# Performance work log

Measured on AMD Instinct MI355X. Metric: run time of the kernel, lower is better.

The kernel has to match this reference:

```python
import jax, jax.numpy as jnp
import numpy as np

D_MODEL = 1024
NHEAD = 16
HEAD_DIM = D_MODEL // NHEAD
MLP_DIM = 4096
ROPE_THETA = 10000.0


def layer_norm(x, g, b, eps=1e-5):
    mu = jnp.mean(x, axis=-1, keepdims=True)
    var = jnp.var(x, axis=-1, keepdims=True)
    return (x - mu) * jax.lax.rsqrt(var + eps) * g + b


def rope_cos_sin(seq_len, dim):
    # lucidrains RotaryEmbedding: inv_freq over even indices, freqs repeated interleaved
    inv_freq = 1.0 / (ROPE_THETA ** (jnp.arange(0, dim, 2, dtype=jnp.float32) / dim))
    t = jnp.arange(seq_len, dtype=jnp.float32)
    freqs = t[:, None] * inv_freq[None, :]            # (S, dim/2)
    freqs = jnp.repeat(freqs, 2, axis=-1)             # (S, dim) interleaved [f0,f0,f1,f1,...]
    return jnp.cos(freqs), jnp.sin(freqs)


def apply_rope(x, cos, sin):
    # x: (B, S, H, D); interleaved rotate_half: (x0,x1) -> (-x1, x0)
    x1 = x[..., ::2]
    x2 = x[..., 1::2]
    rot = jnp.stack([-x2, x1], axis=-1).reshape(x.shape)
    c = cos[None, :, None, :]
    s = sin[None, :, None, :]
    return x * c + rot * s


def setup_inputs() -> dict:
    key = jax.random.key(0)
    ks = jax.random.split(key, 8)
    B, S = 2, 2048
    sc = 1.0 / np.sqrt(D_MODEL)
    inputs = jax.random.normal(ks[0], (B, S, D_MODEL), dtype=jnp.float32)
    return {
        "inputs": inputs,
        "ln1_g": jnp.ones((D_MODEL,), jnp.float32),
        "ln1_b": jnp.zeros((D_MODEL,), jnp.float32),
        "Wq": jax.random.normal(ks[1], (D_MODEL, D_MODEL), jnp.float32) * sc,
        "Wk": jax.random.normal(ks[2], (D_MODEL, D_MODEL), jnp.float32) * sc,
        "Wv": jax.random.normal(ks[3], (D_MODEL, D_MODEL), jnp.float32) * sc,
        "Wo": jax.random.normal(ks[4], (D_MODEL, D_MODEL), jnp.float32) * sc,
        "ln2_g": jnp.ones((D_MODEL,), jnp.float32),
        "ln2_b": jnp.zeros((D_MODEL,), jnp.float32),
        "Wfc2": jax.random.normal(ks[5], (D_MODEL, MLP_DIM), jnp.float32) * sc,
        "bfc2": jnp.zeros((MLP_DIM,), jnp.float32),
        "Wfc3": jax.random.normal(ks[6], (MLP_DIM, D_MODEL), jnp.float32) * (1.0 / np.sqrt(MLP_DIM)),
        "bfc3": jnp.zeros((D_MODEL,), jnp.float32),
    }


def reference(inputs, ln1_g, ln1_b, Wq, Wk, Wv, Wo, ln2_g, ln2_b, Wfc2, bfc2, Wfc3, bfc3):
    B, S, _ = inputs.shape
    x = layer_norm(inputs, ln1_g, ln1_b)
    q = (x @ Wq).reshape(B, S, NHEAD, HEAD_DIM)
    k = (x @ Wk).reshape(B, S, NHEAD, HEAD_DIM)
    v = (x @ Wv).reshape(B, S, NHEAD, HEAD_DIM)
    cos, sin = rope_cos_sin(S, HEAD_DIM)
    q = apply_rope(q, cos, sin)
    k = apply_rope(k, cos, sin)
    scores = jnp.einsum('bqhd,bkhd->bhqk', q, k) / np.sqrt(HEAD_DIM)
    attn = jax.nn.softmax(scores, axis=-1)
    out = jnp.einsum('bhqk,bkhd->bqhd', attn, v).reshape(B, S, D_MODEL)
    out = out @ Wo
    mlp_in = out + inputs
    h = layer_norm(mlp_in, ln2_g, ln2_b)
    h = jax.nn.gelu(h @ Wfc2 + bfc2, approximate=False)
    h = h @ Wfc3 + bfc3
    return h + mlp_in
```

## Files before the change

kernel.cpp:

```cpp
#include <hip/hip_runtime.h>
#include <cstdint>
#include <cstddef>

typedef __bf16 bf16x8 __attribute__((ext_vector_type(8)));
typedef __bf16 bf16x4 __attribute__((ext_vector_type(4)));
typedef float  f32x4  __attribute__((ext_vector_type(4)));
typedef float  f32x16 __attribute__((ext_vector_type(16)));
typedef unsigned int u32x4 __attribute__((ext_vector_type(4)));

__device__ __forceinline__ void load16_to_lds(const void* g, void* l) {
  __builtin_amdgcn_global_load_lds(
      (const __attribute__((address_space(1))) void*)g,
      (__attribute__((address_space(3))) void*)l, 16, 0, 0);
}

__device__ __forceinline__ unsigned cvt_pk_bf16(float a, float b) {
  unsigned r;
  asm("v_cvt_pk_bf16_f32 %0, %1, %2" : "=v"(r) : "v"(a), "v"(b));
  return r;
}
__device__ __forceinline__ void permlane32_swap(unsigned &a, unsigned &b) {
  asm("v_permlane32_swap_b32 %0, %1" : "+v"(a), "+v"(b));
}

__global__ __launch_bounds__(256) void transpose_cast(
    const float* __restrict__ src, __bf16* __restrict__ dst, int K, int N)
{
  __shared__ float tile[32][33];
  const int n0 = blockIdx.x * 32, k0 = blockIdx.y * 32;
  const int tx = threadIdx.x, ty = threadIdx.y;
#pragma unroll
  for (int i = 0; i < 32; i += 8)
    tile[ty + i][tx] = src[(size_t)(k0 + ty + i) * N + n0 + tx];
  __syncthreads();
#pragma unroll
  for (int i = 0; i < 32; i += 8)
    dst[(size_t)(n0 + ty + i) * K + k0 + tx] = (__bf16)tile[tx][ty + i];
}

__global__ __launch_bounds__(256) void transpose_cast_qkv(
    const float* __restrict__ s0, const float* __restrict__ s1,
    const float* __restrict__ s2, __bf16* __restrict__ dst)
{
  __shared__ float tile[32][33];
  const float* src = blockIdx.z == 0 ? s0 : blockIdx.z == 1 ? s1 : s2;
  __bf16* d = dst + (size_t)blockIdx.z * 1024 * 1024;
  const int n0 = blockIdx.x * 32, k0 = blockIdx.y * 32;
  const int tx = threadIdx.x, ty = threadIdx.y;
#pragma unroll
  for (int i = 0; i < 32; i += 8)
    tile[ty + i][tx] = src[(size_t)(k0 + ty + i) * 1024 + n0 + tx];
  __syncthreads();
#pragma unroll
  for (int i = 0; i < 32; i += 8)
    d[(size_t)(n0 + ty + i) * 1024 + k0 + tx] = (__bf16)tile[tx][ty + i];
}

__global__ __launch_bounds__(256) void ln_kernel(
    const float* __restrict__ x, const float* __restrict__ g,
    const float* __restrict__ bta, __bf16* __restrict__ out)
{
  const int row = blockIdx.x;
  const int t = threadIdx.x;
  const float4 v = ((const float4*)(x + (size_t)row * 1024))[t];
  float s  = v.x + v.y + v.z + v.w;
  float ss = v.x * v.x + v.y * v.y + v.z * v.z + v.w * v.w;
#pragma unroll
  for (int o = 32; o > 0; o >>= 1) { s += __shfl_down(s, o); ss += __shfl_down(ss, o); }
  __shared__ float rs[4], rss[4];
  const int w = t >> 6, l = t & 63;
  if (l == 0) { rs[w] = s; rss[w] = ss; }
  __syncthreads();
  s  = rs[0] + rs[1] + rs[2] + rs[3];
  ss = rss[0] + rss[1] + rss[2] + rss[3];
  const float mu = s * (1.0f / 1024.0f);
  const float var = ss * (1.0f / 1024.0f) - mu * mu;
  const float rstd = rsqrtf(var + 1e-5f);
  const float4 gg = ((const float4*)g)[t];
  const float4 bb = ((const float4*)bta)[t];
  __bf16* o = out + (size_t)row * 1024 + t * 4;
  o[0] = (__bf16)((v.x - mu) * rstd * gg.x + bb.x);
  o[1] = (__bf16)((v.y - mu) * rstd * gg.y + bb.y);
  o[2] = (__bf16)((v.z - mu) * rstd * gg.z + bb.z);
  o[3] = (__bf16)((v.w - mu) * rstd * gg.w + bb.w);
}

enum { EPI_BF16 = 0, EPI_RES_F32 = 1, EPI_GELU_BF16 = 2, EPI_BIAS_RES_F32 = 3 };

template <int TM, int KB, int EPI>
__global__ __launch_bounds__(256, 2) void gemm_bf16(
    const __bf16* __restrict__ A, const __bf16* __restrict__ Bt,
    __bf16* __restrict__ outb, float* __restrict__ outf,
    const float* __restrict__ bias, const float* __restrict__ res,
    int M, int N, int K)
{
  constexpr int MT = TM / 32;
  constexpr int KS = KB / 32;
  __shared__ __bf16 As0[TM * KB], As1[TM * KB];
  __shared__ __bf16 Bs0[128 * KB], Bs1[128 * KB];
  const int tid  = threadIdx.x;
  const int lane = tid & 63, w = tid >> 6;
  const int wm = w >> 1, wn = w & 1;
  const int quad = lane >> 4, l16 = lane & 15;
  const int m0 = blockIdx.y * TM, n0 = blockIdx.x * 128;

  f32x4 acc[MT][4] = {};
  const __bf16* Ag = A  + (size_t)m0 * K;
  const __bf16* Bg = Bt + (size_t)n0 * K;

#define G_STAGE(AsX, BsX, k0) {                                            \
    _Pragma("unroll")                                                      \
    for (int r2 = 0; r2 < TM * KB / 2048; ++r2) {                          \
      const int c = r2 * 256 + tid;                                        \
      const int r = c / (KB / 8), cb = c % (KB / 8);                       \
      const int g = (KB == 64) ? (cb ^ (r & 7)) : cb;                      \
      load16_to_lds(Ag + (size_t)r * K + (k0) + g * 8, &AsX[c * 8]);       \
    }                                                                      \
    _Pragma("unroll")                                                      \
    for (int r2 = 0; r2 < KB / 16; ++r2) {                                 \
      const int c = r2 * 256 + tid;                                        \
      const int r = c / (KB / 8), cb = c % (KB / 8);                       \
      const int g = (KB == 64) ? (cb ^ (r & 7)) : cb;                      \
      load16_to_lds(Bg + (size_t)r * K + (k0) + g * 8, &BsX[c * 8]);       \
    } }

#define G_COMPUTE(AsX, BsX) {                                              \
    bf16x8 af[MT][KS], bfr[4][KS];                                         \
    _Pragma("unroll")                                                      \
    for (int mt = 0; mt < MT; ++mt) {                                      \
      const int row = wm * (TM / 2) + mt * 16 + l16;                       \
      _Pragma("unroll")                                                    \
      for (int ks = 0; ks < KS; ++ks) {                                    \
        const int ch = (KB == 64) ? ((ks * 4 + quad) ^ (row & 7)) : quad;  \
        af[mt][ks] = *(const bf16x8*)&AsX[row * KB + ch * 8];              \
      }                                                                    \
    }                                                                      \
    _Pragma("unroll")                                                      \
    for (int nt = 0; nt < 4; ++nt) {                                       \
      const int row = wn * 64 + nt * 16 + l16;                             \
      _Pragma("unroll")                                                    \
      for (int ks = 0; ks < KS; ++ks) {                                    \
        const int ch = (KB == 64) ? ((ks * 4 + quad) ^ (row & 7)) : quad;  \
        bfr[nt][ks] = *(const bf16x8*)&BsX[row * KB + ch * 8];             \
      }                                                                    \
    }                                                                      \
    _Pragma("unroll")                                                      \
    for (int ks = 0; ks < KS; ++ks)                                        \
      _Pragma("unroll")                                                    \
      for (int mt = 0; mt < MT; ++mt)                                      \
        _Pragma("unroll")                                                  \
        for (int nt = 0; nt < 4; ++nt)                                     \
          acc[mt][nt] = __builtin_amdgcn_mfma_f32_16x16x32_bf16(           \
              af[mt][ks], bfr[nt][ks], acc[mt][nt], 0, 0, 0);              \
  }

  G_STAGE(As0, Bs0, 0);
  const int nk = K / KB;
  for (int kt = 0; kt < nk; kt += 2) {
    __syncthreads();
    if (kt + 1 < nk) G_STAGE(As1, Bs1, (kt + 1) * KB);
    G_COMPUTE(As0, Bs0);
    __syncthreads();
    if (kt + 2 < nk) G_STAGE(As0, Bs0, (kt + 2) * KB);
    G_COMPUTE(As1, Bs1);
  }
#undef G_STAGE
#undef G_COMPUTE

#pragma unroll
  for (int mt = 0; mt < MT; ++mt) {
#pragma unroll
    for (int nt = 0; nt < 4; ++nt) {
      const int col = n0 + wn * 64 + nt * 16 + l16;
#pragma unroll
      for (int i = 0; i < 4; ++i) {
        const int row = m0 + wm * (TM / 2) + mt * 16 + quad * 4 + i;
        float v = acc[mt][nt][i];
        const size_t idx = (size_t)row * N + col;
        if (EPI == EPI_BF16) {
          outb[idx] = (__bf16)v;
        } else if (EPI == EPI_RES_F32) {
          outf[idx] = v + res[idx];
        } else if (EPI == EPI_GELU_BF16) {
          v += bias[col];
          outb[idx] = (__bf16)(0.5f * v * (1.0f + erff(v * 0.70710678118f)));
        } else {
          v += bias[col];
          outf[idx] = v + res[idx];
        }
      }
    }
  }
}

__global__ __launch_bounds__(256) void rope_qk(
    const __bf16* __restrict__ qkv, __bf16* __restrict__ qr, __bf16* __restrict__ kr)
{
  const int idx = blockIdx.x * 256 + threadIdx.x;
  const int d2 = idx & 31;
  const int h  = (idx >> 5) & 15;
  const int bs = idx >> 9;
  const int s  = bs & 2047;
  const int b  = bs >> 11;
  const float inv_freq = exp2f(-((float)d2 * (1.0f / 32.0f)) * 13.2877123795f);
  const float ang = (float)s * inv_freq;
  const float c = cosf(ang), sn = sinf(ang);
  const float QS = 0.125f * 1.44269504f;
  const __bf16* qp = qkv + (size_t)bs * 3072 + h * 64 + 2 * d2;
  const __bf16* kp = qp + 1024;
  const float q0 = (float)qp[0], q1 = (float)qp[1];
  const float k0 = (float)kp[0], k1 = (float)kp[1];
  const size_t o = ((size_t)(b * 16 + h) * 2048 + s) * 64 + 2 * d2;
  qr[o]     = (__bf16)((q0 * c - q1 * sn) * QS);
  qr[o + 1] = (__bf16)((q1 * c + q0 * sn) * QS);
  kr[o]     = (__bf16)(k0 * c - k1 * sn);
  kr[o + 1] = (__bf16)(k1 * c + k0 * sn);
}

__global__ __launch_bounds__(256) void v_transpose(
    const __bf16* __restrict__ qkv, __bf16* __restrict__ vt)
{
  __shared__ __bf16 t[64][66];
  const int st = blockIdx.x, h = blockIdx.y, b = blockIdx.z;
  const int tx = threadIdx.x & 63, ty = threadIdx.x >> 6;
  const int s0 = st * 64;
  const __bf16* src = qkv + ((size_t)(b * 2048 + s0)) * 3072 + 2048 + h * 64;
#pragma unroll
  for (int i = 0; i < 64; i += 4)
    t[ty + i][tx] = src[(size_t)(ty + i) * 3072 + tx];
  __syncthreads();
  __bf16* dst = vt + ((size_t)(b * 16 + h) * 64) * 2048 + s0;
#pragma unroll
  for (int i = 0; i < 64; i += 4)
    dst[(size_t)(ty + i) * 2048 + tx] = t[tx][ty + i];
}

__global__ __launch_bounds__(256, 2) void attn_kernel(
    const __bf16* __restrict__ qr, const __bf16* __restrict__ kr,
    const __bf16* __restrict__ vt, __bf16* __restrict__ attn_o)
{
  constexpr int S = 2048, DH = 64, NH = 16, BQ = 128, BKK = 64;
  __shared__ __align__(16) __bf16 Qs[BQ * 64];
  __shared__ __align__(16) __bf16 Ks0[64 * 64], Ks1[64 * 64], Ks2[64 * 64], Ks3[64 * 64];
  __shared__ __align__(16) __bf16 Vts0[64 * 64], Vts1[64 * 64], Vts2[64 * 64], Vts3[64 * 64];

  const int tid = threadIdx.x;
  const int lane = tid & 63, w = tid >> 6;
  const int l32 = lane & 31, half = lane >> 5;
  const int qt = blockIdx.x, h = blockIdx.y, b = blockIdx.z;
  const int bh = b * NH + h;
  const __bf16* Q  = qr + ((size_t)bh * S + qt * BQ) * DH;
  const __bf16* Kp = kr + (size_t)bh * S * DH;
  const __bf16* Vp = vt + (size_t)bh * DH * S;
  __bf16* Pb = Qs + w * 2048;

#define A_STAGE(KsX, VtsX, kk) {                                           \
    _Pragma("unroll")                                                      \
    for (int r2 = 0; r2 < 2; ++r2) {                                       \
      const int c = r2 * 256 + tid;                                        \
      const int r = c >> 3, cb = c & 7;                                    \
      const int cg = (cb ^ (r & 7)) * 8;                                   \
      load16_to_lds(Kp + (size_t)((kk) + r) * DH + cg, &KsX[c * 8]);       \
      load16_to_lds(Vp + (size_t)r * S + (kk) + cg, &VtsX[c * 8]);         \
    } }

#pragma unroll
  for (int r4 = 0; r4 < 4; ++r4) {
    const int c = r4 * 256 + tid;
    const int r = c >> 3, cb = c & 7;
    load16_to_lds(Q + (size_t)r * DH + ((cb ^ (r & 7)) * 8), &Qs[c * 8]);
  }
  A_STAGE(Ks0, Vts0, 0);
  A_STAGE(Ks1, Vts1, BKK);
  __syncthreads();

  bf16x8 qfB[4];
  {
    const int row = w * 32 + l32;
#pragma unroll
    for (int c = 0; c < 4; ++c)
      qfB[c] = *(const bf16x8*)&Qs[row * 64 + (((2 * c + half) ^ (row & 7)) * 8)];
  }

  float mreg = -3.0e38f, lreg = 0.0f;
  f32x16 oacc[2] = {};
  const f32x16 zz = {};
  f32x16 saA[2], saB[2];

#define A_QK(KsX, saX) {                                                   \
    bf16x8 kf[2][4];                                                       \
    _Pragma("unroll")                                                      \
    for (int t = 0; t < 2; ++t) {                                          \
      const int row = 32 * t + l32;                                        \
      _Pragma("unroll")                                                    \
      for (int c = 0; c < 4; ++c)                                          \
        kf[t][c] = *(const bf16x8*)&KsX[row * 64 + (((2 * c + half) ^ (l32 & 7)) * 8)]; \
    }                                                                      \
    __builtin_amdgcn_s_setprio(1);                                         \
    _Pragma("unroll")                                                      \
    for (int t = 0; t < 2; ++t) {                                          \
      saX[t] = __builtin_amdgcn_mfma_f32_32x32x16_bf16(kf[t][0], qfB[0], zz, 0, 0, 0); \
      _Pragma("unroll")                                                    \
      for (int c = 1; c < 4; ++c)                                          \
        saX[t] = __builtin_amdgcn_mfma_f32_32x32x16_bf16(kf[t][c], qfB[c], saX[t], 0, 0, 0); \
    }                                                                      \
    __builtin_amdgcn_s_setprio(0);                                         \
  }

#define A_SMPV(saC, VtsX) {                                                \
    bf16x8 vf[2][4];                                                       \
    _Pragma("unroll")                                                      \
    for (int v = 0; v < 2; ++v) {                                          \
      const int row = 32 * v + l32;                                        \
      _Pragma("unroll")                                                    \
      for (int c = 0; c < 4; ++c)                                          \
        vf[v][c] = *(const bf16x8*)&VtsX[row * 64 + (((2 * c + half) ^ (l32 & 7)) * 8)]; \
    }                                                                      \
    float pm[8];                                                           \
    _Pragma("unroll")                                                      \
    for (int t = 0; t < 2; ++t)                                            \
      _Pragma("unroll")                                                    \
      for (int g = 0; g < 4; ++g)                                          \
        pm[t * 4 + g] = fmaxf(fmaxf(saC[t][4 * g], saC[t][4 * g + 1]),     \
                              fmaxf(saC[t][4 * g + 2], saC[t][4 * g + 3]));\
    float mx = fmaxf(fmaxf(fmaxf(pm[0], pm[1]), fmaxf(pm[2], pm[3])),      \
                     fmaxf(fmaxf(pm[4], pm[5]), fmaxf(pm[6], pm[7])));     \
    mx = fmaxf(mx, __shfl_xor(mx, 32));                                    \
    float mnew = mreg;                                                     \
    if (!__all(mx <= mreg + 8.0f)) {                                       \
      mnew = fmaxf(mreg, mx);                                              \
      const float alpha = __builtin_amdgcn_exp2f(mreg - mnew);             \
      mreg = mnew;                                                         \
      lreg *= alpha;                                                       \
      _Pragma("unroll")                                                    \
      for (int v = 0; v < 2; ++v)                                          \
        _Pragma("unroll")                                                  \
        for (int r = 0; r < 16; ++r) oacc[v][r] *= alpha;                  \
    }                                                                      \
    float ps0 = 0.f, ps1 = 0.f, ps2 = 0.f, ps3 = 0.f;                      \
    _Pragma("unroll")                                                      \
    for (int t = 0; t < 2; ++t)                                            \
      _Pragma("unroll")                                                    \
      for (int r = 0; r < 16; r += 4) {                                    \
        const float p0 = __builtin_amdgcn_exp2f(saC[t][r]     - mnew);     \
        const float p1 = __builtin_amdgcn_exp2f(saC[t][r + 1] - mnew);     \
        const float p2 = __builtin_amdgcn_exp2f(saC[t][r + 2] - mnew);     \
        const float p3 = __builtin_amdgcn_exp2f(saC[t][r + 3] - mnew);     \
        saC[t][r] = p0; saC[t][r + 1] = p1;                                \
        saC[t][r + 2] = p2; saC[t][r + 3] = p3;                            \
        ps0 += p0; ps1 += p1; ps2 += p2; ps3 += p3;                        \
      }                                                                    \
    __builtin_amdgcn_s_setprio(1);                                         \
    _Pragma("unroll")                                                      \
    for (int c = 0; c < 4; ++c) {                                          \
      const int t = c >> 1, r0 = (c & 1) * 8;                              \
      unsigned px = cvt_pk_bf16(saC[t][r0],     saC[t][r0 + 1]);           \
      unsigned py = cvt_pk_bf16(saC[t][r0 + 2], saC[t][r0 + 3]);           \
      unsigned pz = cvt_pk_bf16(saC[t][r0 + 4], saC[t][r0 + 5]);           \
      unsigned pw = cvt_pk_bf16(saC[t][r0 + 6], saC[t][r0 + 7]);           \
      permlane32_swap(px, pz);                                             \
      permlane32_swap(py, pw);                                             \
      const u32x4 pv4 = { px, py, pz, pw };                                \
      const bf16x8 pf = __builtin_bit_cast(bf16x8, pv4);                   \
      oacc[0] = __builtin_amdgcn_mfma_f32_32x32x16_bf16(vf[0][c], pf, oacc[0], 0, 0, 0); \
      oacc[1] = __builtin_amdgcn_mfma_f32_32x32x16_bf16(vf[1][c], pf, oacc[1], 0, 0, 0); \
    }                                                                      \
    __builtin_amdgcn_s_setprio(0);                                         \
    float sum = (ps0 + ps1) + (ps2 + ps3);                                 \
    sum += __shfl_xor(sum, 32);                                            \
    lreg += sum;                                                           \
  }

#define A_PHASE(KsNext, VtsCur, KsSt, VtsSt, saCur, saNext, kkSt, DO_QK, DO_ST) { \
    __syncthreads();                                                       \
    if (DO_ST) A_STAGE(KsSt, VtsSt, kkSt);                                 \
    if (DO_QK) A_QK(KsNext, saNext);                                       \
    A_SMPV(saCur, VtsCur);                                                 \
  }

  A_QK(Ks0, saA);

  for (int p = 0; p < 28; p += 4) {
    A_PHASE(Ks1, Vts0, Ks2, Vts2, saA, saB, (p + 2) * BKK, true, true);
    A_PHASE(Ks2, Vts1, Ks3, Vts3, saB, saA, (p + 3) * BKK, true, true);
    A_PHASE(Ks3, Vts2, Ks0, Vts0, saA, saB, (p + 4) * BKK, true, true);
    A_PHASE(Ks0, Vts3, Ks1, Vts1, saB, saA, (p + 5) * BKK, true, true);
  }
  A_PHASE(Ks1, Vts0, Ks2, Vts2, saA, saB, 30 * BKK, true, true);
  A_PHASE(Ks2, Vts1, Ks3, Vts3, saB, saA, 31 * BKK, true, true);
  A_PHASE(Ks3, Vts2, Ks0, Vts0, saA, saB, 0,        true, false);
  A_PHASE(Ks0, Vts3, Ks1, Vts1, saB, saA, 0,        false, false);
#undef A_STAGE
#undef A_QK
#undef A_SMPV
#undef A_PHASE

  const float linv = 1.0f / lreg;
#pragma unroll
  for (int v = 0; v < 2; ++v)
#pragma unroll
    for (int g = 0; g < 4; ++g) {
      bf16x4 ov;
#pragma unroll
      for (int i = 0; i < 4; ++i) ov[i] = (__bf16)(oacc[v][4 * g + i] * linv);
      const int dc = 4 * v + g;
      *(bf16x4*)&Pb[l32 * 64 + ((dc ^ (l32 & 7)) * 8) + 4 * half] = ov;
    }
#pragma unroll
  for (int cc = 0; cc < 4; ++cc) {
    const int c = cc * 64 + lane;
    const int r = c >> 3, g = c & 7;
    const bf16x8 od = *(const bf16x8*)&Pb[r * 64 + ((g ^ (r & 7)) * 8)];
    const int srow = qt * BQ + w * 32 + r;
    *(bf16x8*)&attn_o[((size_t)b * S + srow) * 1024 + h * 64 + g * 8] = od;
  }
}

extern "C" void kernel_launch(void* const* d_in, const int* in_sizes, int n_in,
                              void* d_out, int out_size, void* d_ws, size_t ws_size,
                              hipStream_t stream) {
  const float* inputs = (const float*)d_in[0];
  const float* ln1_g  = (const float*)d_in[1];
  const float* ln1_b  = (const float*)d_in[2];
  const float* Wq     = (const float*)d_in[3];
  const float* Wk     = (const float*)d_in[4];
  const float* Wv     = (const float*)d_in[5];
  const float* Wo     = (const float*)d_in[6];
  const float* ln2_g  = (const float*)d_in[7];
  const float* ln2_b  = (const float*)d_in[8];
  const float* Wfc2   = (const float*)d_in[9];
  const float* bfc2   = (const float*)d_in[10];
  const float* Wfc3   = (const float*)d_in[11];
  const float* bfc3   = (const float*)d_in[12];
  float* out = (float*)d_out;
  char* ws = (char*)d_ws;
  const size_t MB = 1024 * 1024;

  __bf16* Wqkv_t = (__bf16*)(ws);
  __bf16* Wo_t   = (__bf16*)(ws + 6 * MB);
  __bf16* Wfc2_t = (__bf16*)(ws + 8 * MB);
  __bf16* Wfc3_t = (__bf16*)(ws + 16 * MB);
  __bf16* xb     = (__bf16*)(ws + 24 * MB);
  __bf16* attn_o = xb;
  __bf16* qkv    = (__bf16*)(ws + 32 * MB);
  float*  mlp_in = (float*)(ws + 32 * MB);
  __bf16* h2     = (__bf16*)(ws + 48 * MB);
  __bf16* qrb    = (__bf16*)(ws + 56 * MB);
  __bf16* krb    = (__bf16*)(ws + 64 * MB);
  __bf16* vtb    = (__bf16*)(ws + 72 * MB);
  __bf16* hbuf   = (__bf16*)(ws + 56 * MB);

  const dim3 tb(32, 8);
  transpose_cast_qkv<<<dim3(32, 32, 3), tb, 0, stream>>>(Wq, Wk, Wv, Wqkv_t);
  transpose_cast<<<dim3(32, 32),  tb, 0, stream>>>(Wo,   Wo_t,   1024, 1024);
  transpose_cast<<<dim3(128, 32), tb, 0, stream>>>(Wfc2, Wfc2_t, 1024, 4096);
  transpose_cast<<<dim3(32, 128), tb, 0, stream>>>(Wfc3, Wfc3_t, 4096, 1024);

  ln_kernel<<<4096, 256, 0, stream>>>(inputs, ln1_g, ln1_b, xb);

  gemm_bf16<128, 64, EPI_BF16><<<dim3(24, 32), 256, 0, stream>>>(
      xb, Wqkv_t, qkv, nullptr, nullptr, nullptr, 4096, 3072, 1024);

  rope_qk<<<8192, 256, 0, stream>>>(qkv, qrb, krb);
  v_transpose<<<dim3(32, 16, 2), 256, 0, stream>>>(qkv, vtb);

  attn_kernel<<<dim3(16, 16, 2), 256, 0, stream>>>(qrb, krb, vtb, attn_o);

  gemm_bf16<64, 64, EPI_RES_F32><<<dim3(8, 64), 256, 0, stream>>>(
      attn_o, Wo_t, nullptr, mlp_in, nullptr, inputs, 4096, 1024, 1024);

  ln_kernel<<<4096, 256, 0, stream>>>(mlp_in, ln2_g, ln2_b, h2);

  gemm_bf16<128, 64, EPI_GELU_BF16><<<dim3(32, 32), 256, 0, stream>>>(
      h2, Wfc2_t, hbuf, nullptr, bfc2, nullptr, 4096, 4096, 1024);

  gemm_bf16<64, 64, EPI_BIAS_RES_F32><<<dim3(8, 64), 256, 0, stream>>>(
      hbuf, Wfc3_t, nullptr, out, bfc3, mlp_in, 4096, 1024, 4096);
}
```

Before: 348.1 us.

## Add 256x256-tile 512-thread GEMM for QKV and FC2 projections

Adds a new bf16 MFMA GEMM kernel with 256x256 output tiles, 8 waves per block, double-buffered XOR-swizzled LDS staging via global_load_lds, and BF16 or GELU epilogues. The QKV and FC2 GEMMs switch from 128x64 tiles to this kernel to raise data reuse per LDS load and cut global traffic. The larger tiles use 128KB of LDS per block and produce far fewer blocks (192 for QKV, 256 for FC2). That risks leaving CUs idle and losing latency hiding from multiple resident blocks.

```diff
diff --git a/kernel.cpp b/kernel.cpp
--- a/kernel.cpp
+++ b/kernel.cpp
@@ -187,6 +187,99 @@
         } else {
           v += bias[col];
           outf[idx] = v + res[idx];
+        }
+      }
+    }
+  }
+}
+
+template <int EPI>
+__global__ __launch_bounds__(512, 2) void gemm_bf16_256(
+    const __bf16* __restrict__ A, const __bf16* __restrict__ Bt,
+    __bf16* __restrict__ outb, float* __restrict__ outf,
+    const float* __restrict__ bias, const float* __restrict__ res,
+    int M, int N, int K)
+{
+  __shared__ __bf16 As0[256 * 64], As1[256 * 64];
+  __shared__ __bf16 Bs0[256 * 64], Bs1[256 * 64];
+  const int tid  = threadIdx.x;
+  const int lane = tid & 63, w = tid >> 6;
+  const int wm = w >> 2, wn = w & 3;
+  const int quad = lane >> 4, l16 = lane & 15;
+  const int m0 = blockIdx.y * 256, n0 = blockIdx.x * 256;
+
+  f32x4 acc[8][4] = {};
+  const __bf16* Ag = A  + (size_t)m0 * K;
+  const __bf16* Bg = Bt + (size_t)n0 * K;
+
+#define GB_STAGE(AsX, BsX, k0) {                                           \
+    _Pragma("unroll")                                                      \
+    for (int r2 = 0; r2 < 4; ++r2) {                                       \
+      const int c = r2 * 512 + tid;                                        \
+      const int r = c >> 3, cb = c & 7;                                    \
+      const int g = cb ^ (r & 7);                                          \
+      load16_to_lds(Ag + (size_t)r * K + (k0) + g * 8, &AsX[c * 8]);       \
+    }                                                                      \
+    _Pragma("unroll")                                                      \
+    for (int r2 = 0; r2 < 4; ++r2) {                                       \
+      const int c = r2 * 512 + tid;                                        \
+      const int r = c >> 3, cb = c & 7;                                    \
+      const int g = cb ^ (r & 7);                                          \
+      load16_to_lds(Bg + (size_t)r * K + (k0) + g * 8, &BsX[c * 8]);       \
+    } }
+
+#define GB_COMPUTE(AsX, BsX) {                                             \
+    _Pragma("unroll")                                                      \
+    for (int ks = 0; ks < 2; ++ks) {                                       \
+      bf16x8 af[8], bfr[4];                                                \
+      _Pragma("unroll")                                                    \
+      for (int mt = 0; mt < 8; ++mt) {                                     \
+        const int row = wm * 128 + mt * 16 + l16;                          \
+        const int ch = (ks * 4 + quad) ^ (row & 7);                        \
+        af[mt] = *(const bf16x8*)&AsX[row * 64 + ch * 8];                  \
+      }                                                                    \
+      _Pragma("unroll")                                                    \
+      for (int nt = 0; nt < 4; ++nt) {                                     \
+        const int row = wn * 64 + nt * 16 + l16;                           \
+        const int ch = (ks * 4 + quad) ^ (row & 7);                        \
+        bfr[nt] = *(const bf16x8*)&BsX[row * 64 + ch * 8];                 \
+      }                                                                    \
+      _Pragma("unroll")                                                    \
+      for (int mt = 0; mt < 8; ++mt)                                       \
+        _Pragma("unroll")                                                  \
+        for (int nt = 0; nt < 4; ++nt)                                     \
+          acc[mt][nt] = __builtin_amdgcn_mfma_f32_16x16x32_bf16(           \
+              af[mt], bfr[nt], acc[mt][nt], 0, 0, 0);                      \
+    } }
+
+  GB_STAGE(As0, Bs0, 0);
+  const int nk = K / 64;
+  for (int kt = 0; kt < nk; kt += 2) {
+    __syncthreads();
+    if (kt + 1 < nk) GB_STAGE(As1, Bs1, (kt + 1) * 64);
+    GB_COMPUTE(As0, Bs0);
+    __syncthreads();
+    if (kt + 2 < nk) GB_STAGE(As0, Bs0, (kt + 2) * 64);
+    GB_COMPUTE(As1, Bs1);
+  }
+#undef GB_STAGE
+#undef GB_COMPUTE
+
+#pragma unroll
+  for (int mt = 0; mt < 8; ++mt) {
+#pragma unroll
+    for (int nt = 0; nt < 4; ++nt) {
+      const int col = n0 + wn * 64 + nt * 16 + l16;
+#pragma unroll
+      for (int i = 0; i < 4; ++i) {
+        const int row = m0 + wm * 128 + mt * 16 + quad * 4 + i;
+        float v = acc[mt][nt][i];
+        const size_t idx = (size_t)row * N + col;
+        if (EPI == EPI_BF16) {
+          outb[idx] = (__bf16)v;
+        } else if (EPI == EPI_GELU_BF16) {
+          v += bias[col];
+          outb[idx] = (__bf16)(0.5f * v * (1.0f + erff(v * 0.70710678118f)));
         }
       }
     }
@@ -458,7 +551,7 @@
 
   ln_kernel<<<4096, 256, 0, stream>>>(inputs, ln1_g, ln1_b, xb);
 
-  gemm_bf16<128, 64, EPI_BF16><<<dim3(24, 32), 256, 0, stream>>>(
+  gemm_bf16_256<EPI_BF16><<<dim3(12, 16), 512, 0, stream>>>(
       xb, Wqkv_t, qkv, nullptr, nullptr, nullptr, 4096, 3072, 1024);
 
   rope_qk<<<8192, 256, 0, stream>>>(qkv, qrb, krb);
@@ -471,7 +564,7 @@
 
   ln_kernel<<<4096, 256, 0, stream>>>(mlp_in, ln2_g, ln2_b, h2);
 
-  gemm_bf16<128, 64, EPI_GELU_BF16><<<dim3(32, 32), 256, 0, stream>>>(
+  gemm_bf16_256<EPI_GELU_BF16><<<dim3(16, 16), 512, 0, stream>>>(
       h2, Wfc2_t, hbuf, nullptr, bfc2, nullptr, 4096, 4096, 1024);
 
   gemm_bf16<64, 64, EPI_BIAS_RES_F32><<<dim3(8, 64), 256, 0, stream>>>(
```

Result: no change. 348.6 us (+0.2%).

## Add 256x256-tile 4-stage pipelined GEMM for QKV and FC2 projections

Applied to the files above, without the earlier changes.

Introduces a new GEMM kernel with 256x256 output tiles, 512 threads and a four-buffer LDS ring fed by direct global-to-LDS loads with counted vmcnt waits. It replaces the 128x64 GEMM for the QKV projection and the GELU FC2 projection. Larger tiles raise arithmetic intensity per loaded byte and the deeper prefetch hides memory latency. The cost is fewer blocks (192 and 256 workgroups on 256 CUs), which leaves some CUs idle or underfilled, plus a large register footprint at one block per CU.

```diff
diff --git a/kernel.cpp b/kernel.cpp
--- a/kernel.cpp
+++ b/kernel.cpp
@@ -187,6 +187,103 @@
         } else {
           v += bias[col];
           outf[idx] = v + res[idx];
+        }
+      }
+    }
+  }
+}
+
+template <int EPI>
+__global__ __launch_bounds__(512, 1) void gemm_bf16_256p(
+    const __bf16* __restrict__ A, const __bf16* __restrict__ Bt,
+    __bf16* __restrict__ outb, const float* __restrict__ bias,
+    int M, int N, int K)
+{
+  __shared__ __bf16 As0[256 * 32], As1[256 * 32], As2[256 * 32], As3[256 * 32];
+  __shared__ __bf16 Bs0[256 * 32], Bs1[256 * 32], Bs2[256 * 32], Bs3[256 * 32];
+  const int tid  = threadIdx.x;
+  const int lane = tid & 63, w = tid >> 6;
+  const int wm = w >> 2, wn = w & 3;
+  const int quad = lane >> 4, l16 = lane & 15;
+  const int m0 = blockIdx.y * 256, n0 = blockIdx.x * 256;
+
+  f32x4 acc[8][4] = {};
+  const __bf16* Ag = A  + (size_t)m0 * K;
+  const __bf16* Bg = Bt + (size_t)n0 * K;
+
+#define P_STAGE(AsX, BsX, t) {                                             \
+    const int k0 = (t) * 32;                                               \
+    _Pragma("unroll")                                                      \
+    for (int r2 = 0; r2 < 2; ++r2) {                                       \
+      const int c = r2 * 512 + tid;                                        \
+      const int r = c >> 2, cb = c & 3;                                    \
+      load16_to_lds(Ag + (size_t)r * K + k0 + cb * 8, &AsX[c * 8]);        \
+    }                                                                      \
+    _Pragma("unroll")                                                      \
+    for (int r2 = 0; r2 < 2; ++r2) {                                       \
+      const int c = r2 * 512 + tid;                                        \
+      const int r = c >> 2, cb = c & 3;                                    \
+      load16_to_lds(Bg + (size_t)r * K + k0 + cb * 8, &BsX[c * 8]);        \
+    } }
+
+#define P_COMPUTE(AsX, BsX) {                                              \
+    bf16x8 af[8], bfr[4];                                                  \
+    _Pragma("unroll")                                                      \
+    for (int mt = 0; mt < 8; ++mt)                                         \
+      af[mt] = *(const bf16x8*)&AsX[(wm * 128 + mt * 16 + l16) * 32 + quad * 8]; \
+    _Pragma("unroll")                                                      \
+    for (int nt = 0; nt < 4; ++nt)                                         \
+      bfr[nt] = *(const bf16x8*)&BsX[(wn * 64 + nt * 16 + l16) * 32 + quad * 8]; \
+    __builtin_amdgcn_s_setprio(1);                                         \
+    _Pragma("unroll")                                                      \
+    for (int mt = 0; mt < 8; ++mt)                                         \
+      _Pragma("unroll")                                                    \
+      for (int nt = 0; nt < 4; ++nt)                                       \
+        acc[mt][nt] = __builtin_amdgcn_mfma_f32_16x16x32_bf16(             \
+            af[mt], bfr[nt], acc[mt][nt], 0, 0, 0);                        \
+    __builtin_amdgcn_s_setprio(0);                                         \
+  }
+
+#define P_WAITBAR(NTOK) {                                                  \
+    asm volatile("s_waitcnt vmcnt(" NTOK ")" ::: "memory");                \
+    __builtin_amdgcn_s_barrier();                                          \
+    asm volatile("" ::: "memory");                                         \
+  }
+
+  P_STAGE(As0, Bs0, 0);
+  P_STAGE(As1, Bs1, 1);
+  P_STAGE(As2, Bs2, 2);
+  const int nk = K / 32;
+  int kt = 0;
+  for (; kt + 8 <= nk; kt += 4) {
+    P_WAITBAR("8");  P_STAGE(As3, Bs3, kt + 3);  P_COMPUTE(As0, Bs0);
+    P_WAITBAR("8");  P_STAGE(As0, Bs0, kt + 4);  P_COMPUTE(As1, Bs1);
+    P_WAITBAR("8");  P_STAGE(As1, Bs1, kt + 5);  P_COMPUTE(As2, Bs2);
+    P_WAITBAR("8");  P_STAGE(As2, Bs2, kt + 6);  P_COMPUTE(As3, Bs3);
+  }
+  P_WAITBAR("8");  P_STAGE(As3, Bs3, kt + 3);  P_COMPUTE(As0, Bs0);
+  P_WAITBAR("8");  P_COMPUTE(As1, Bs1);
+  P_WAITBAR("4");  P_COMPUTE(As2, Bs2);
+  P_WAITBAR("0");  P_COMPUTE(As3, Bs3);
+#undef P_STAGE
+#undef P_COMPUTE
+#undef P_WAITBAR
+
+#pragma unroll
+  for (int mt = 0; mt < 8; ++mt) {
+#pragma unroll
+    for (int nt = 0; nt < 4; ++nt) {
+      const int col = n0 + wn * 64 + nt * 16 + l16;
+#pragma unroll
+      for (int i = 0; i < 4; ++i) {
+        const int row = m0 + wm * 128 + mt * 16 + quad * 4 + i;
+        float v = acc[mt][nt][i];
+        const size_t idx = (size_t)row * N + col;
+        if (EPI == EPI_BF16) {
+          outb[idx] = (__bf16)v;
+        } else if (EPI == EPI_GELU_BF16) {
+          v += bias[col];
+          outb[idx] = (__bf16)(0.5f * v * (1.0f + erff(v * 0.70710678118f)));
         }
       }
     }
@@ -458,8 +555,8 @@
 
   ln_kernel<<<4096, 256, 0, stream>>>(inputs, ln1_g, ln1_b, xb);
 
-  gemm_bf16<128, 64, EPI_BF16><<<dim3(24, 32), 256, 0, stream>>>(
-      xb, Wqkv_t, qkv, nullptr, nullptr, nullptr, 4096, 3072, 1024);
+  gemm_bf16_256p<EPI_BF16><<<dim3(12, 16), 512, 0, stream>>>(
+      xb, Wqkv_t, qkv, nullptr, 4096, 3072, 1024);
 
   rope_qk<<<8192, 256, 0, stream>>>(qkv, qrb, krb);
   v_transpose<<<dim3(32, 16, 2), 256, 0, stream>>>(qkv, vtb);
@@ -471,8 +568,8 @@
 
   ln_kernel<<<4096, 256, 0, stream>>>(mlp_in, ln2_g, ln2_b, h2);
 
-  gemm_bf16<128, 64, EPI_GELU_BF16><<<dim3(32, 32), 256, 0, stream>>>(
-      h2, Wfc2_t, hbuf, nullptr, bfc2, nullptr, 4096, 4096, 1024);
+  gemm_bf16_256p<EPI_GELU_BF16><<<dim3(16, 16), 512, 0, stream>>>(
+      h2, Wfc2_t, hbuf, bfc2, 4096, 4096, 1024);
 
   gemm_bf16<64, 64, EPI_BIAS_RES_F32><<<dim3(8, 64), 256, 0, stream>>>(
       hbuf, Wfc3_t, nullptr, out, bfc3, mlp_in, 4096, 1024, 4096);
```

Result: no change. 352.6 us (+1.3%).

## Fuse RoPE into QKV GEMM epilogue and shrink K-block for 128-row GEMMs

Applied to the files above, without the earlier changes.

Removes the standalone rope_qk kernel. The QKV GEMM epilogue now applies the rotary rotation directly, taking each element's pair partner from the neighbouring lane with a shuffle, and writes Q and K in head-major layout. V still goes through the bf16 qkv buffer. This saves one kernel launch and a full read-back of Q and K. The 128-row GEMMs also drop their K-block size from 64 to 32, which halves shared memory and may raise occupancy at the cost of more synchronisation per k-step. The epilogue now computes sin and cos per element and does scattered 2-byte stores.

```diff
diff --git a/kernel.cpp b/kernel.cpp
--- a/kernel.cpp
+++ b/kernel.cpp
@@ -85,13 +85,15 @@
   o[3] = (__bf16)((v.w - mu) * rstd * gg.w + bb.w);
 }
 
-enum { EPI_BF16 = 0, EPI_RES_F32 = 1, EPI_GELU_BF16 = 2, EPI_BIAS_RES_F32 = 3 };
+enum { EPI_BF16 = 0, EPI_RES_F32 = 1, EPI_GELU_BF16 = 2, EPI_BIAS_RES_F32 = 3,
+       EPI_QKV_ROPE = 4 };
 
 template <int TM, int KB, int EPI>
 __global__ __launch_bounds__(256, 2) void gemm_bf16(
     const __bf16* __restrict__ A, const __bf16* __restrict__ Bt,
     __bf16* __restrict__ outb, float* __restrict__ outf,
     const float* __restrict__ bias, const float* __restrict__ res,
+    __bf16* __restrict__ qrp, __bf16* __restrict__ krp,
     int M, int N, int K)
 {
   constexpr int MT = TM / 32;
@@ -184,37 +186,33 @@
         } else if (EPI == EPI_GELU_BF16) {
           v += bias[col];
           outb[idx] = (__bf16)(0.5f * v * (1.0f + erff(v * 0.70710678118f)));
-        } else {
+        } else if (EPI == EPI_BIAS_RES_F32) {
           v += bias[col];
           outf[idx] = v + res[idx];
+        } else {
+          const float vp = __shfl_xor(v, 1);
+          const int role = col >> 10;
+          if (role == 2) {
+            outb[idx] = (__bf16)v;
+          } else {
+            const int s  = row & 2047, bb = row >> 11;
+            const int cl = col & 1023;
+            const int hh = cl >> 6, d = cl & 63, d2 = d >> 1;
+            const float inv_freq =
+                exp2f(-((float)d2 * (1.0f / 32.0f)) * 13.2877123795f);
+            const float ang = (float)s * inv_freq;
+            const float cs = cosf(ang), sn = sinf(ang);
+            const float rot = (d & 1) ? (v * cs + vp * sn) : (v * cs - vp * sn);
+            const size_t o = ((size_t)(bb * 16 + hh) * 2048 + s) * 64 + d;
+            if (role == 0)
+              qrp[o] = (__bf16)(rot * (0.125f * 1.44269504f));
+            else
+              krp[o] = (__bf16)rot;
+          }
         }
       }
     }
   }
-}
-
-__global__ __launch_bounds__(256) void rope_qk(
-    const __bf16* __restrict__ qkv, __bf16* __restrict__ qr, __bf16* __restrict__ kr)
-{
-  const int idx = blockIdx.x * 256 + threadIdx.x;
-  const int d2 = idx & 31;
-  const int h  = (idx >> 5) & 15;
-  const int bs = idx >> 9;
-  const int s  = bs & 2047;
-  const int b  = bs >> 11;
-  const float inv_freq = exp2f(-((float)d2 * (1.0f / 32.0f)) * 13.2877123795f);
-  const float ang = (float)s * inv_freq;
-  const float c = cosf(ang), sn = sinf(ang);
-  const float QS = 0.125f * 1.44269504f;
-  const __bf16* qp = qkv + (size_t)bs * 3072 + h * 64 + 2 * d2;
-  const __bf16* kp = qp + 1024;
-  const float q0 = (float)qp[0], q1 = (float)qp[1];
-  const float k0 = (float)kp[0], k1 = (float)kp[1];
-  const size_t o = ((size_t)(b * 16 + h) * 2048 + s) * 64 + 2 * d2;
-  qr[o]     = (__bf16)((q0 * c - q1 * sn) * QS);
-  qr[o + 1] = (__bf16)((q1 * c + q0 * sn) * QS);
-  kr[o]     = (__bf16)(k0 * c - k1 * sn);
-  kr[o + 1] = (__bf16)(k1 * c + k0 * sn);
 }
 
 __global__ __launch_bounds__(256) void v_transpose(
@@ -458,22 +456,24 @@
 
   ln_kernel<<<4096, 256, 0, stream>>>(inputs, ln1_g, ln1_b, xb);
 
-  gemm_bf16<128, 64, EPI_BF16><<<dim3(24, 32), 256, 0, stream>>>(
-      xb, Wqkv_t, qkv, nullptr, nullptr, nullptr, 4096, 3072, 1024);
-
-  rope_qk<<<8192, 256, 0, stream>>>(qkv, qrb, krb);
+  gemm_bf16<128, 32, EPI_QKV_ROPE><<<dim3(24, 32), 256, 0, stream>>>(
+      xb, Wqkv_t, qkv, nullptr, nullptr, nullptr, qrb, krb, 4096, 3072, 1024);
+
   v_transpose<<<dim3(32, 16, 2), 256, 0, stream>>>(qkv, vtb);
 
   attn_kernel<<<dim3(16, 16, 2), 256, 0, stream>>>(qrb, krb, vtb, attn_o);
 
   gemm_bf16<64, 64, EPI_RES_F32><<<dim3(8, 64), 256, 0, stream>>>(
-      attn_o, Wo_t, nullptr, mlp_in, nullptr, inputs, 4096, 1024, 1024);
+      attn_o, Wo_t, nullptr, mlp_in, nullptr, inputs, nullptr, nullptr,
+      4096, 1024, 1024);
 
   ln_kernel<<<4096, 256, 0, stream>>>(mlp_in, ln2_g, ln2_b, h2);
 
-  gemm_bf16<128, 64, EPI_GELU_BF16><<<dim3(32, 32), 256, 0, stream>>>(
-      h2, Wfc2_t, hbuf, nullptr, bfc2, nullptr, 4096, 4096, 1024);
+  gemm_bf16<128, 32, EPI_GELU_BF16><<<dim3(32, 32), 256, 0, stream>>>(
+      h2, Wfc2_t, hbuf, nullptr, bfc2, nullptr, nullptr, nullptr,
+      4096, 4096, 1024);
 
   gemm_bf16<64, 64, EPI_BIAS_RES_F32><<<dim3(8, 64), 256, 0, stream>>>(
-      hbuf, Wfc3_t, nullptr, out, bfc3, mlp_in, 4096, 1024, 4096);
-}
+      hbuf, Wfc3_t, nullptr, out, bfc3, mlp_in, nullptr, nullptr,
+      4096, 1024, 4096);
+}
```

After: 809.5 us. 133% more time.
